# Performance work log

Hardware: AMD Instinct MI355X
Metric: run time of the kernel (lower is better)

## Reference

```python
import jax, jax.numpy as jnp
import numpy as np

K = 2          # kernel_size
STRIDE = 1
C_IN = 2       # n_channels (hardcoded in module)
NQ = K * K     # 4 qubits
PI = np.pi


def _apply_1q(state, gate, wire):
    # state: [N, 16] complex64; gate: [N,2,2] (batched) or [2,2] (shared)
    N = state.shape[0]
    s = state.reshape((N,) + (2,) * NQ)
    s = jnp.moveaxis(s, 1 + wire, NQ)          # wire axis -> last
    s = s.reshape(N, -1, 2)
    if gate.ndim == 3:
        s = jnp.einsum('nab,nkb->nka', gate, s)
    else:
        s = jnp.einsum('ab,nkb->nka', gate, s)
    s = s.reshape((N,) + (2,) * NQ)
    s = jnp.moveaxis(s, NQ, 1 + wire)
    return s.reshape(N, -1)


def _apply_cnot(state, ctrl, tgt):
    N = state.shape[0]
    s = state.reshape((N,) + (2,) * NQ)
    s = jnp.moveaxis(s, (1 + ctrl, 1 + tgt), (NQ - 1, NQ))
    shp = s.shape
    s = s.reshape(N, -1, 2, 2)                 # [..., ctrl, tgt]
    s = jnp.concatenate([s[:, :, :1, :], s[:, :, 1:, ::-1]], axis=2)
    s = s.reshape(shp)
    s = jnp.moveaxis(s, (NQ - 1, NQ), (1 + ctrl, 1 + tgt))
    return s.reshape(N, -1)


def _rx(theta):
    # theta: [N] or scalar -> [N,2,2] or [2,2] complex
    c = jnp.cos(theta / 2).astype(jnp.complex64)
    s = (-1j) * jnp.sin(theta / 2).astype(jnp.complex64)
    return jnp.stack([jnp.stack([c, s], -1), jnp.stack([s, c], -1)], -2)


def _ry(theta):
    c = jnp.cos(theta / 2)
    s = jnp.sin(theta / 2)
    return jnp.stack([jnp.stack([c, -s], -1), jnp.stack([s, c], -1)], -2).astype(jnp.complex64)


def _circuit(angles, weights):
    # angles: [N, 8]; weights: [L, 4]. Returns expval(PauliZ) per wire: [N, 4].
    N = angles.shape[0]
    state = jnp.zeros((N, 2 ** NQ), jnp.complex64).at[:, 0].set(1.0)
    for i in range(NQ):
        state = _apply_1q(state, _rx(angles[:, 2 * i]), i)
        state = _apply_1q(state, _ry(angles[:, 2 * i + 1]), i)
    # BasicEntanglerLayers: per layer RX(w[l,i]) on wire i, then CNOT ring
    for l in range(weights.shape[0]):
        for i in range(NQ):
            state = _apply_1q(state, _rx(weights[l, i]), i)
        for i in range(NQ):
            state = _apply_cnot(state, i, (i + 1) % NQ)
    p = state.real ** 2 + state.imag ** 2
    p = p.reshape((N,) + (2,) * NQ)
    ez = [jnp.sum(jnp.take(p, 0, axis=1 + w) - jnp.take(p, 1, axis=1 + w),
                  axis=tuple(range(1, NQ))) for w in range(NQ)]
    return jnp.stack(ez, -1)


def _forward(x, weights):
    B, C, H, W = x.shape
    nh = (H - K) // STRIDE + 1
    nw = (W - K) // STRIDE + 1
    # unfold: [B, C, nh, nw, K*K] with patch-element order (kh, kw)
    subs = [x[:, :, kh:kh + (nh - 1) * STRIDE + 1:STRIDE,
                    kw:kw + (nw - 1) * STRIDE + 1:STRIDE]
            for kh in range(K) for kw in range(K)]
    patches = jnp.stack(subs, axis=-1)                      # [B,C,nh,nw,KK]
    patches = patches.transpose(0, 2, 3, 4, 1)              # [B,nh,nw,KK,C]
    patches = patches.reshape(B, nh * nw, K * K * C)
    # per-sample min-max normalize to [0, pi]
    flat = patches.reshape(B, -1)
    pmin = flat.min(axis=1)[:, None, None]
    pmax = flat.max(axis=1)[:, None, None]
    angles = (patches - pmin) / (pmax - pmin + 1e-8) * PI
    angles = angles.reshape(B * nh * nw, K * K * C)
    out = _circuit(angles, weights)                         # [B*nh*nw, 4]
    return out.reshape(B, nh, nw, NQ).transpose(0, 3, 1, 2)


def setup_inputs() -> dict:
    key = jax.random.key(0)
    k1, k2 = jax.random.split(key)
    x = jax.random.normal(k1, (8, C_IN, 224, 224), dtype=jnp.float32)
    weights = jax.random.uniform(k2, (1, NQ), dtype=jnp.float32) * (2 * PI)
    return {"x": x, "weights": weights}


def reference(x, weights):
    return _forward(x, weights)
```

## Files before the change

### kernel.cpp

```cpp
#include <hip/hip_runtime.h>
#include <math.h>

#define BATCH 8
#define CIN   2
#define H     224
#define W     224
#define NH    223
#define NW    223
#define PIXB  (H * W)
#define NPB   (CIN * H * W)
#define PER_B (NH * NW)
#define NBPB  ((PER_B + 255) / 256)
#define BPB   32
#define PI_F  3.14159265358979323846f

__global__ __launch_bounds__(256) void minmax_kernel(
        const float* __restrict__ x, float* __restrict__ ws) {
    int b  = blockIdx.x / BPB;
    int cb = blockIdx.x % BPB;
    const float4* xb = (const float4*)(x + (size_t)b * NPB);
    const int n4  = NPB / 4;
    const int per = n4 / BPB;
    float lmin =  INFINITY, lmax = -INFINITY;
    for (int idx = cb * per + threadIdx.x; idx < (cb + 1) * per; idx += 256) {
        float4 v = xb[idx];
        lmin = fminf(lmin, fminf(fminf(v.x, v.y), fminf(v.z, v.w)));
        lmax = fmaxf(lmax, fmaxf(fmaxf(v.x, v.y), fmaxf(v.z, v.w)));
    }
    #pragma unroll
    for (int off = 32; off > 0; off >>= 1) {
        lmin = fminf(lmin, __shfl_down(lmin, off, 64));
        lmax = fmaxf(lmax, __shfl_down(lmax, off, 64));
    }
    __shared__ float smin[4], smax[4];
    int wid = threadIdx.x >> 6;
    if ((threadIdx.x & 63) == 0) { smin[wid] = lmin; smax[wid] = lmax; }
    __syncthreads();
    if (threadIdx.x == 0) {
        #pragma unroll
        for (int i = 1; i < 4; ++i) {
            lmin = fminf(lmin, smin[i]);
            lmax = fmaxf(lmax, smax[i]);
        }
        ws[b * BPB + cb]               = lmin;
        ws[256 + b * BPB + cb]         = lmax;
    }
}

__global__ __launch_bounds__(256) void quanv_kernel(
        const float* __restrict__ x, const float* __restrict__ wts,
        const float* __restrict__ ws, float* __restrict__ out) {
    int b = blockIdx.y;
    __shared__ float sred[2];
    if (threadIdx.x < 32) {
        float mn = ws[b * BPB + threadIdx.x];
        float mx = ws[256 + b * BPB + threadIdx.x];
        #pragma unroll
        for (int off = 16; off > 0; off >>= 1) {
            mn = fminf(mn, __shfl_xor(mn, off, 32));
            mx = fmaxf(mx, __shfl_xor(mx, off, 32));
        }
        if (threadIdx.x == 0) { sred[0] = mn; sred[1] = mx; }
    }
    __syncthreads();
    float gmin  = sred[0];
    float scale = PI_F / (sred[1] - gmin + 1e-8f);

    int r = blockIdx.x * 256 + threadIdx.x;
    if (r >= PER_B) return;
    int i = r / NW;
    int j = r - i * NW;

    const float* c0 = x + (size_t)b * NPB + (size_t)i * W + j;
    const float* c1 = c0 + PIXB;

    float z[4];
    #pragma unroll
    for (int q = 0; q < 4; ++q) {
        int kh = q >> 1, kw = q & 1;
        float pa = c0[kh * W + kw];
        float pb = c1[kh * W + kw];
        float a  = (pa - gmin) * scale;
        float bb = (pb - gmin) * scale;
        float sa, ca;
        __sincosf(a, &sa, &ca);
        float cb = __cosf(bb);
        float sw, cw;
        __sincosf(wts[q], &sw, &cw);
        z[q] = ca * cb * cw - sa * sw;
    }

    size_t base = (size_t)b * 4 * PER_B + r;
    float z01 = z[0] * z[1];
    out[base]             = z[1] * z[2] * z[3];
    out[base + PER_B]     = z01;
    out[base + 2 * PER_B] = z01 * z[2];
    out[base + 3 * PER_B] = z01 * z[2] * z[3];
}

extern "C" void kernel_launch(void* const* d_in, const int* in_sizes, int n_in,
                              void* d_out, int out_size, void* d_ws, size_t ws_size,
                              hipStream_t stream) {
    const float* x   = (const float*)d_in[0];
    const float* wts = (const float*)d_in[1];
    float* out = (float*)d_out;
    float* ws  = (float*)d_ws;

    minmax_kernel<<<BATCH * BPB, 256, 0, stream>>>(x, ws);
    quanv_kernel<<<dim3(NBPB, BATCH), 256, 0, stream>>>(x, wts, ws, out);
}
```

Measured before the change: 61.69 us.

## Fuse min-max reduction and quanv into one cooperative kernel with grid sync

Replaces the two-kernel pipeline (min-max reduction, then per-patch circuit evaluation) with a single cooperative kernel. Each of 64x8 blocks computes a partial min/max, a grid-wide sync publishes them, and the blocks then grid-stride over the output patches. Weight sin/cos is hoisted out of the per-patch loop. This removes one kernel launch and the gap between the kernels, but adds grid-sync cost and caps the main phase at 512 blocks, which limits parallelism. The old two-kernel path is kept as a fallback if the cooperative launch fails.

```diff
diff --git a/kernel.cpp b/kernel.cpp
--- a/kernel.cpp
+++ b/kernel.cpp
@@ -1,4 +1,5 @@
 #include <hip/hip_runtime.h>
+#include <hip/hip_cooperative_groups.h>
 #include <math.h>
 
 #define BATCH 8
@@ -10,17 +11,104 @@
 #define PIXB  (H * W)
 #define NPB   (CIN * H * W)
 #define PER_B (NH * NW)
+#define GBX   64
+#define N4    (NPB / 4)
+#define PERBLK (N4 / GBX)
+#define PI_F  3.14159265358979323846f
+
+namespace cg = cooperative_groups;
+
+__global__ __launch_bounds__(256) void fused_quanv(
+        const float* __restrict__ x, const float* __restrict__ wts,
+        float* __restrict__ ws, float* __restrict__ out) {
+    const int b  = blockIdx.y;
+    const int cb = blockIdx.x;
+
+    const float4* xb = (const float4*)(x + (size_t)b * NPB);
+    float lmin =  INFINITY, lmax = -INFINITY;
+    for (int idx = cb * PERBLK + threadIdx.x; idx < (cb + 1) * PERBLK; idx += 256) {
+        float4 v = xb[idx];
+        lmin = fminf(lmin, fminf(fminf(v.x, v.y), fminf(v.z, v.w)));
+        lmax = fmaxf(lmax, fmaxf(fmaxf(v.x, v.y), fmaxf(v.z, v.w)));
+    }
+    #pragma unroll
+    for (int off = 32; off > 0; off >>= 1) {
+        lmin = fminf(lmin, __shfl_down(lmin, off, 64));
+        lmax = fmaxf(lmax, __shfl_down(lmax, off, 64));
+    }
+    __shared__ float smin[4], smax[4];
+    const int wid = threadIdx.x >> 6;
+    if ((threadIdx.x & 63) == 0) { smin[wid] = lmin; smax[wid] = lmax; }
+    __syncthreads();
+    if (threadIdx.x == 0) {
+        #pragma unroll
+        for (int i = 1; i < 4; ++i) {
+            lmin = fminf(lmin, smin[i]);
+            lmax = fmaxf(lmax, smax[i]);
+        }
+        ws[b * GBX + cb]               = lmin;
+        ws[BATCH * GBX + b * GBX + cb] = lmax;
+    }
+
+    cg::this_grid().sync();
+
+    __shared__ float sred[2];
+    if (threadIdx.x < GBX) {
+        float mn = ws[b * GBX + threadIdx.x];
+        float mx = ws[BATCH * GBX + b * GBX + threadIdx.x];
+        #pragma unroll
+        for (int off = 32; off > 0; off >>= 1) {
+            mn = fminf(mn, __shfl_down(mn, off, 64));
+            mx = fmaxf(mx, __shfl_down(mx, off, 64));
+        }
+        if (threadIdx.x == 0) { sred[0] = mn; sred[1] = mx; }
+    }
+    __syncthreads();
+    const float gmin  = sred[0];
+    const float scale = PI_F / (sred[1] - gmin + 1e-8f);
+
+    float sw[4], cw[4];
+    #pragma unroll
+    for (int q = 0; q < 4; ++q) __sincosf(wts[q], &sw[q], &cw[q]);
+
+    const float* xbase = x + (size_t)b * NPB;
+    const size_t obase = (size_t)b * 4 * PER_B;
+
+    for (int r = cb * 256 + threadIdx.x; r < PER_B; r += GBX * 256) {
+        int i = r / NW;
+        int j = r - i * NW;
+        const float* c0 = xbase + i * W + j;
+        const float* c1 = c0 + PIXB;
+
+        float z[4];
+        #pragma unroll
+        for (int q = 0; q < 4; ++q) {
+            int kh = q >> 1, kw = q & 1;
+            float a  = (c0[kh * W + kw] - gmin) * scale;
+            float bb = (c1[kh * W + kw] - gmin) * scale;
+            float sa, ca;
+            __sincosf(a, &sa, &ca);
+            float cb2 = __cosf(bb);
+            z[q] = ca * cb2 * cw[q] - sa * sw[q];
+        }
+
+        float z01 = z[0] * z[1];
+        out[obase + r]             = z[1] * z[2] * z[3];
+        out[obase + PER_B + r]     = z01;
+        out[obase + 2 * PER_B + r] = z01 * z[2];
+        out[obase + 3 * PER_B + r] = z01 * z[2] * z[3];
+    }
+}
+
+#define BPB   32
 #define NBPB  ((PER_B + 255) / 256)
-#define BPB   32
-#define PI_F  3.14159265358979323846f
 
 __global__ __launch_bounds__(256) void minmax_kernel(
         const float* __restrict__ x, float* __restrict__ ws) {
     int b  = blockIdx.x / BPB;
     int cb = blockIdx.x % BPB;
     const float4* xb = (const float4*)(x + (size_t)b * NPB);
-    const int n4  = NPB / 4;
-    const int per = n4 / BPB;
+    const int per = (NPB / 4) / BPB;
     float lmin =  INFINITY, lmax = -INFINITY;
     for (int idx = cb * per + threadIdx.x; idx < (cb + 1) * per; idx += 256) {
         float4 v = xb[idx];
@@ -42,8 +130,8 @@
             lmin = fminf(lmin, smin[i]);
             lmax = fmaxf(lmax, smax[i]);
         }
-        ws[b * BPB + cb]               = lmin;
-        ws[256 + b * BPB + cb]         = lmax;
+        ws[b * BPB + cb]       = lmin;
+        ws[256 + b * BPB + cb] = lmax;
     }
 }
 
@@ -85,9 +173,9 @@
         float sa, ca;
         __sincosf(a, &sa, &ca);
         float cb = __cosf(bb);
-        float sw, cw;
-        __sincosf(wts[q], &sw, &cw);
-        z[q] = ca * cb * cw - sa * sw;
+        float sw, cwv;
+        __sincosf(wts[q], &sw, &cwv);
+        z[q] = ca * cb * cwv - sa * sw;
     }
 
     size_t base = (size_t)b * 4 * PER_B + r;
@@ -106,6 +194,12 @@
     float* out = (float*)d_out;
     float* ws  = (float*)d_ws;
 
-    minmax_kernel<<<BATCH * BPB, 256, 0, stream>>>(x, ws);
-    quanv_kernel<<<dim3(NBPB, BATCH), 256, 0, stream>>>(x, wts, ws, out);
-}
+    void* args[] = { (void*)&x, (void*)&wts, (void*)&ws, (void*)&out };
+    dim3 grid(GBX, BATCH), block(256, 1, 1);
+    hipError_t err = hipLaunchCooperativeKernel(
+        (const void*)fused_quanv, grid, block, args, 0, stream);
+    if (err != hipSuccess) {
+        minmax_kernel<<<BATCH * BPB, 256, 0, stream>>>(x, ws);
+        quanv_kernel<<<dim3(NBPB, BATCH), 256, 0, stream>>>(x, wts, ws, out);
+    }
+}
```

Result: slower. 104.9 us (+70.1%).

## Process four output columns per thread with float4 loads and shared trig

Applied to the files above, without the earlier changes.

Each thread in the quanv kernel now handles four adjacent output positions. It loads float4 rows plus one extra element and computes each input pixel's sin/cos once, then reuses it for the overlapping 2x2 patches, so trig work and load instructions per output drop. The weight sin/cos is also precomputed once in the minmax kernel and read from the workspace instead of being recomputed in every thread. In exchange, the output stores are no longer perfectly coalesced (each thread writes four consecutive floats), register use is higher, and there are fewer threads in flight.

```diff
diff --git a/kernel.cpp b/kernel.cpp
--- a/kernel.cpp
+++ b/kernel.cpp
@@ -10,17 +10,26 @@
 #define PIXB  (H * W)
 #define NPB   (CIN * H * W)
 #define PER_B (NH * NW)
-#define NBPB  ((PER_B + 255) / 256)
 #define BPB   32
+#define TPR   56
+#define SLOTS (NH * TPR)
+#define QBLK  ((SLOTS + 255) / 256)
 #define PI_F  3.14159265358979323846f
 
+
 __global__ __launch_bounds__(256) void minmax_kernel(
-        const float* __restrict__ x, float* __restrict__ ws) {
+        const float* __restrict__ x, const float* __restrict__ wts,
+        float* __restrict__ ws) {
+    if (blockIdx.x == 0 && threadIdx.x < 4) {
+        float s, c;
+        __sincosf(wts[threadIdx.x], &s, &c);
+        ws[512 + threadIdx.x] = s;
+        ws[516 + threadIdx.x] = c;
+    }
     int b  = blockIdx.x / BPB;
     int cb = blockIdx.x % BPB;
     const float4* xb = (const float4*)(x + (size_t)b * NPB);
-    const int n4  = NPB / 4;
-    const int per = n4 / BPB;
+    const int per = (NPB / 4) / BPB;
     float lmin =  INFINITY, lmax = -INFINITY;
     for (int idx = cb * per + threadIdx.x; idx < (cb + 1) * per; idx += 256) {
         float4 v = xb[idx];
@@ -42,15 +51,15 @@
             lmin = fminf(lmin, smin[i]);
             lmax = fmaxf(lmax, smax[i]);
         }
-        ws[b * BPB + cb]               = lmin;
-        ws[256 + b * BPB + cb]         = lmax;
+        ws[b * BPB + cb]       = lmin;
+        ws[256 + b * BPB + cb] = lmax;
     }
 }
 
 __global__ __launch_bounds__(256) void quanv_kernel(
-        const float* __restrict__ x, const float* __restrict__ wts,
-        const float* __restrict__ ws, float* __restrict__ out) {
-    int b = blockIdx.y;
+        const float* __restrict__ x, const float* __restrict__ ws,
+        float* __restrict__ out) {
+    const int b = blockIdx.y;
     __shared__ float sred[2];
     if (threadIdx.x < 32) {
         float mn = ws[b * BPB + threadIdx.x];
@@ -63,39 +72,58 @@
         if (threadIdx.x == 0) { sred[0] = mn; sred[1] = mx; }
     }
     __syncthreads();
-    float gmin  = sred[0];
-    float scale = PI_F / (sred[1] - gmin + 1e-8f);
+    const float gmin  = sred[0];
+    const float scale = PI_F / (sred[1] - gmin + 1e-8f);
 
-    int r = blockIdx.x * 256 + threadIdx.x;
-    if (r >= PER_B) return;
-    int i = r / NW;
-    int j = r - i * NW;
+    const float sw0 = ws[512], sw1 = ws[513], sw2 = ws[514], sw3 = ws[515];
+    const float cw0 = ws[516], cw1 = ws[517], cw2 = ws[518], cw3 = ws[519];
 
-    const float* c0 = x + (size_t)b * NPB + (size_t)i * W + j;
-    const float* c1 = c0 + PIXB;
+    int slot = blockIdx.x * 256 + threadIdx.x;
+    if (slot >= SLOTS) return;
+    int i  = slot / TPR;
+    int jt = (slot - i * TPR) * 4;
+    const int npos = (jt == 220) ? 3 : 4;
 
-    float z[4];
+    const float* r0 = x + (size_t)b * NPB + i * W + jt;
+    const float* r1 = r0 + W;
+    const float* r2 = r0 + PIXB;
+    const float* r3 = r2 + W;
+    float4 v0 = *(const float4*)r0;
+    float4 v1 = *(const float4*)r1;
+    float4 v2 = *(const float4*)r2;
+    float4 v3 = *(const float4*)r3;
+    float e0 = 0.f, e1 = 0.f, e2 = 0.f, e3 = 0.f;
+    if (jt < 220) { e0 = r0[4]; e1 = r1[4]; e2 = r2[4]; e3 = r3[4]; }
+
+    const float p0[5] = {v0.x, v0.y, v0.z, v0.w, e0};
+    const float p1[5] = {v1.x, v1.y, v1.z, v1.w, e1};
+    const float p2[5] = {v2.x, v2.y, v2.z, v2.w, e2};
+    const float p3[5] = {v3.x, v3.y, v3.z, v3.w, e3};
+
+    float sa0[5], ca0[5], sa1[5], ca1[5], cb0[5], cb1[5];
     #pragma unroll
-    for (int q = 0; q < 4; ++q) {
-        int kh = q >> 1, kw = q & 1;
-        float pa = c0[kh * W + kw];
-        float pb = c1[kh * W + kw];
-        float a  = (pa - gmin) * scale;
-        float bb = (pb - gmin) * scale;
-        float sa, ca;
-        __sincosf(a, &sa, &ca);
-        float cb = __cosf(bb);
-        float sw, cw;
-        __sincosf(wts[q], &sw, &cw);
-        z[q] = ca * cb * cw - sa * sw;
+    for (int k = 0; k < 5; ++k) {
+        __sincosf((p0[k] - gmin) * scale, &sa0[k], &ca0[k]);
+        __sincosf((p1[k] - gmin) * scale, &sa1[k], &ca1[k]);
+        cb0[k] = __cosf((p2[k] - gmin) * scale);
+        cb1[k] = __cosf((p3[k] - gmin) * scale);
     }
 
-    size_t base = (size_t)b * 4 * PER_B + r;
-    float z01 = z[0] * z[1];
-    out[base]             = z[1] * z[2] * z[3];
-    out[base + PER_B]     = z01;
-    out[base + 2 * PER_B] = z01 * z[2];
-    out[base + 3 * PER_B] = z01 * z[2] * z[3];
+    const size_t obase = (size_t)b * 4 * PER_B + (size_t)i * NW + jt;
+    #pragma unroll
+    for (int p = 0; p < 4; ++p) {
+        if (p < npos) {
+            float z0 = ca0[p]     * cb0[p]     * cw0 - sa0[p]     * sw0;
+            float z1 = ca0[p + 1] * cb0[p + 1] * cw1 - sa0[p + 1] * sw1;
+            float z2 = ca1[p]     * cb1[p]     * cw2 - sa1[p]     * sw2;
+            float z3 = ca1[p + 1] * cb1[p + 1] * cw3 - sa1[p + 1] * sw3;
+            float z01 = z0 * z1;
+            out[obase + p]             = z1 * z2 * z3;
+            out[obase + PER_B + p]     = z01;
+            out[obase + 2 * PER_B + p] = z01 * z2;
+            out[obase + 3 * PER_B + p] = z01 * z2 * z3;
+        }
+    }
 }
 
 extern "C" void kernel_launch(void* const* d_in, const int* in_sizes, int n_in,
@@ -106,6 +134,6 @@
     float* out = (float*)d_out;
     float* ws  = (float*)d_ws;
 
-    minmax_kernel<<<BATCH * BPB, 256, 0, stream>>>(x, ws);
-    quanv_kernel<<<dim3(NBPB, BATCH), 256, 0, stream>>>(x, wts, ws, out);
+    minmax_kernel<<<BATCH * BPB, 256, 0, stream>>>(x, wts, ws);
+    quanv_kernel<<<dim3(QBLK, BATCH), 256, 0, stream>>>(x, ws, out);
 }
```

New measurement: 62.51 us. No clear change (+1.3%).
